# Kernel optimization log

Hardware: AMD Instinct MI355X
Metric: run time of the kernel (lower is better)

The kernel has to match this reference:

```python
import jax, jax.numpy as jnp
import numpy as np

N_NODES = 100000
N_EDGES = 1600000
IN_FEATS = 128
N_HIDDEN = 128
OUT_DIM = 32
BN_EPS = 1e-5


def setup_inputs() -> dict:
    key = jax.random.key(0)
    ks = jax.random.split(key, 12)
    s = 0.05  # weight init scale
    return {
        "features": jax.random.normal(ks[0], (N_NODES, IN_FEATS), dtype=jnp.float32),
        "src": jax.random.randint(ks[1], (N_EDGES,), 0, N_NODES),
        "dst": jax.random.randint(ks[2], (N_EDGES,), 0, N_NODES),
        # layer 0: in_feats -> n_hidden
        "Ws0": jax.random.normal(ks[3], (IN_FEATS, N_HIDDEN), dtype=jnp.float32) * s,
        "Wn0": jax.random.normal(ks[4], (IN_FEATS, N_HIDDEN), dtype=jnp.float32) * s,
        "b0": jnp.zeros((N_HIDDEN,), jnp.float32),
        # layer 1: n_hidden -> n_hidden
        "Ws1": jax.random.normal(ks[5], (N_HIDDEN, N_HIDDEN), dtype=jnp.float32) * s,
        "Wn1": jax.random.normal(ks[6], (N_HIDDEN, N_HIDDEN), dtype=jnp.float32) * s,
        "b1": jnp.zeros((N_HIDDEN,), jnp.float32),
        # layer 2 (output): n_hidden -> out_dim, no activation
        "Ws2": jax.random.normal(ks[7], (N_HIDDEN, OUT_DIM), dtype=jnp.float32) * s,
        "Wn2": jax.random.normal(ks[8], (N_HIDDEN, OUT_DIM), dtype=jnp.float32) * s,
        "b2": jnp.zeros((OUT_DIM,), jnp.float32),
        # batch norms after layers 0 and 1
        "g0": jnp.ones((N_HIDDEN,), jnp.float32),
        "be0": jnp.zeros((N_HIDDEN,), jnp.float32),
        "g1": jnp.ones((N_HIDDEN,), jnp.float32),
        "be1": jnp.zeros((N_HIDDEN,), jnp.float32),
    }


def _sage_mean(h, src, dst, inv_deg, Ws, Wn, b):
    # DGL SAGEConv('mean'): fc_self(h) + fc_neigh(mean of in-neighbor feats)
    agg = jax.ops.segment_sum(h[src], dst, num_segments=N_NODES) * inv_deg
    return h @ Ws + agg @ Wn + b


def _batch_norm(h, gamma, beta):
    mu = jnp.mean(h, axis=0)
    var = jnp.var(h, axis=0)
    return (h - mu) * jax.lax.rsqrt(var + BN_EPS) * gamma + beta


def reference(features, src, dst, Ws0, Wn0, b0, Ws1, Wn1, b1, Ws2, Wn2, b2, g0, be0, g1, be1):
    ones = jnp.ones((N_EDGES,), jnp.float32)
    deg = jax.ops.segment_sum(ones, dst, num_segments=N_NODES)
    inv_deg = (1.0 / jnp.maximum(deg, 1.0))[:, None]  # [N,1]

    # layer 0: SAGEConv internal activation, then BN + external activation
    h = jax.nn.relu(_sage_mean(features, src, dst, inv_deg, Ws0, Wn0, b0))
    h = jax.nn.relu(_batch_norm(h, g0, be0))
    # layer 1 (hidden)
    h = jax.nn.relu(_sage_mean(h, src, dst, inv_deg, Ws1, Wn1, b1))
    h = jax.nn.relu(_batch_norm(h, g1, be1))
    # layer 2 (output): no activation, no BN (idx > n_hidden_layers)
    h = _sage_mean(h, src, dst, inv_deg, Ws2, Wn2, b2)

    # dgl.mean_nodes over a single graph -> [1, out_dim], then softmax over classes
    hg = jnp.mean(h, axis=0, keepdims=True)
    return jax.nn.softmax(hg, axis=1)
```

## Files before the change

kernel.cpp:

```cpp
#include <hip/hip_runtime.h>
#include <hip/hip_bf16.h>

typedef __hip_bfloat16 bf16;
typedef __hip_bfloat162 bf162;

#define NN 100000
#define NE 1600000
#define BN_EPS 1e-5f

#define BSH 8
#define NBUCK ((NN + 255) >> BSH)
#define ABLK 128
#define EPBA ((NE + ABLK - 1) / ABLK)
#define CAP 6144

struct alignas(16) bf16x8 { bf16 v[8]; };

typedef __bf16 bfrag __attribute__((ext_vector_type(8)));
typedef float f4 __attribute__((ext_vector_type(4)));
typedef float f16v __attribute__((ext_vector_type(16)));
typedef float f2 __attribute__((ext_vector_type(2)));

static __device__ __forceinline__ float b2f(bf16 x){ return __bfloat162float(x); }
static __device__ __forceinline__ bf16 f2b(float x){ return __float2bfloat16(x); }

static __device__ __forceinline__ uint2 pk8_fp8(float x0,float x1,float x2,float x3,
                                                float x4,float x5,float x6,float x7)
{
    int lo = __builtin_amdgcn_cvt_pk_fp8_f32(x0, x1, 0, 0);
    lo = __builtin_amdgcn_cvt_pk_fp8_f32(x2, x3, lo, 1);
    int hi = __builtin_amdgcn_cvt_pk_fp8_f32(x4, x5, 0, 0);
    hi = __builtin_amdgcn_cvt_pk_fp8_f32(x6, x7, hi, 1);
    return make_uint2((unsigned)lo, (unsigned)hi);
}

__global__ __launch_bounds__(256) void k_convert(const float* __restrict__ in,
                                                 unsigned char* __restrict__ outf8, int n)
{
    int i = (blockIdx.x * 256 + threadIdx.x) * 8;
    if (i + 7 < n) {
        float4 a = *(const float4*)(in + i);
        float4 b = *(const float4*)(in + i + 4);
        *(uint2*)(outf8 + i) = pk8_fp8(a.x,a.y,a.z,a.w,b.x,b.y,b.z,b.w);
    }
}

__global__ __launch_bounds__(256) void k_wtrans(const float* __restrict__ W0, const float* __restrict__ W1,
                                                const float* __restrict__ W2, const float* __restrict__ W3,
                                                bf16* __restrict__ T0, bf16* __restrict__ T1,
                                                bf16* __restrict__ T2, bf16* __restrict__ T3)
{
    int m = blockIdx.x >> 6;
    int t = (blockIdx.x & 63) * 256 + threadIdx.x;
    const float* W = (m == 0) ? W0 : (m == 1) ? W1 : (m == 2) ? W2 : W3;
    bf16* T = (m == 0) ? T0 : (m == 1) ? T1 : (m == 2) ? T2 : T3;
    int j = t & 7;
    int lane = (t >> 3) & 63;
    int frag = t >> 9;
    int ks = frag >> 2, ct = frag & 3;
    int k = ks * 16 + (lane >> 5) * 8 + j;
    int n = ct * 32 + (lane & 31);
    T[t] = f2b(W[k * 128 + n]);
}

__global__ __launch_bounds__(256) void k_pa1(const int* __restrict__ dst, const int* __restrict__ src,
                                             int* __restrict__ bucketCountD, int* __restrict__ blockBaseD,
                                             int* __restrict__ bucketCountS, int* __restrict__ blockBaseS)
{
    __shared__ int histD[NBUCK];
    __shared__ int histS[NBUCK];
    int t = threadIdx.x;
    for (int i = t; i < NBUCK; i += 256) { histD[i] = 0; histS[i] = 0; }
    __syncthreads();
    int e0 = blockIdx.x * EPBA, e1 = min(e0 + EPBA, NE);
    for (int e = e0 + t; e < e1; e += 256) {
        unsigned bd = ((unsigned)dst[e]) >> BSH;
        unsigned bs = ((unsigned)src[e]) >> BSH;
        if (bd < (unsigned)NBUCK) atomicAdd(&histD[bd], 1);
        if (bs < (unsigned)NBUCK) atomicAdd(&histS[bs], 1);
    }
    __syncthreads();
    for (int i = t; i < NBUCK; i += 256) {
        blockBaseD[blockIdx.x * NBUCK + i] = atomicAdd(&bucketCountD[i], histD[i]);
        blockBaseS[blockIdx.x * NBUCK + i] = atomicAdd(&bucketCountS[i], histS[i]);
    }
}

__global__ __launch_bounds__(512) void k_bscan2(const int* __restrict__ cntD, int* __restrict__ startD,
                                                const int* __restrict__ cntS, int* __restrict__ startS)
{
    __shared__ int sd[512];
    const int* cnt = (blockIdx.x == 0) ? cntD : cntS;
    int* start = (blockIdx.x == 0) ? startD : startS;
    int t = threadIdx.x;
    int v = (t < NBUCK) ? cnt[t] : 0;
    sd[t] = v;
    __syncthreads();
    for (int o = 1; o < 512; o <<= 1) {
        int x = (t >= o) ? sd[t - o] : 0;
        __syncthreads();
        sd[t] += x;
        __syncthreads();
    }
    if (t < NBUCK) start[t] = sd[t] - v;
    if (t == 0) start[NBUCK] = NE;
}

__global__ __launch_bounds__(256) void k_pa2(const int* __restrict__ src, const int* __restrict__ dst,
                                             const int* __restrict__ bucketStartD, const int* __restrict__ blockBaseD,
                                             const int* __restrict__ bucketStartS, const int* __restrict__ blockBaseS,
                                             unsigned* __restrict__ packD, unsigned* __restrict__ packS)
{
    __shared__ int baseD[NBUCK];
    __shared__ int curD[NBUCK];
    __shared__ int baseS[NBUCK];
    __shared__ int curS[NBUCK];
    int t = threadIdx.x;
    for (int i = t; i < NBUCK; i += 256) {
        baseD[i] = bucketStartD[i] + blockBaseD[blockIdx.x * NBUCK + i];
        curD[i] = 0;
        baseS[i] = bucketStartS[i] + blockBaseS[blockIdx.x * NBUCK + i];
        curS[i] = 0;
    }
    __syncthreads();
    int e0 = blockIdx.x * EPBA, e1 = min(e0 + EPBA, NE);
    for (int e = e0 + t; e < e1; e += 256) {
        int s = src[e], d = dst[e];
        unsigned bd = ((unsigned)d) >> BSH;
        if (bd < (unsigned)NBUCK) {
            int r = atomicAdd(&curD[bd], 1);
            unsigned idx = (unsigned)(baseD[bd] + r);
            if (idx < (unsigned)NE)
                packD[idx] = (((unsigned)d & 255u) << 24) | ((unsigned)s & 0xFFFFFFu);
        }
        unsigned bs = ((unsigned)s) >> BSH;
        if (bs < (unsigned)NBUCK) {
            int r = atomicAdd(&curS[bs], 1);
            unsigned idx = (unsigned)(baseS[bs] + r);
            if (idx < (unsigned)NE)
                packS[idx] = (((unsigned)s & 255u) << 24) | ((unsigned)d & 0xFFFFFFu);
        }
    }
}

__global__ __launch_bounds__(256) void k_pbD(const unsigned* __restrict__ packD, const int* __restrict__ bucketStartD,
                                             int* __restrict__ offs, float* __restrict__ invd,
                                             int* __restrict__ esrc)
{
    __shared__ int dcnt[256];
    __shared__ int sscan[256];
    __shared__ int cur[256];
    __shared__ int S[CAP];
    int t = threadIdx.x;
    int b = blockIdx.x;
    int base = b << BSH;
    dcnt[t] = 0;
    cur[t] = 0;
    for (int i = t; i < CAP; i += 256) S[i] = 0;
    __syncthreads();
    int p0 = bucketStartD[b], p1 = bucketStartD[b + 1];
    int cnt = p1 - p0;
    for (int i = p0 + t; i < p1; i += 256)
        atomicAdd(&dcnt[packD[i] >> 24], 1);
    __syncthreads();
    int my = dcnt[t];
    sscan[t] = my;
    __syncthreads();
    for (int o = 1; o < 256; o <<= 1) {
        int v = (t >= o) ? sscan[t - o] : 0;
        __syncthreads();
        sscan[t] += v;
        __syncthreads();
    }
    int lo = sscan[t] - my;
    if (base + t < NN) {
        offs[base + t] = p0 + lo;
        invd[base + t] = 1.0f / (float)max(my, 1);
    }
    if (b == NBUCK - 1 && t == 0) offs[NN] = NE;
    __syncthreads();
    sscan[t] = lo;
    __syncthreads();
    if (cnt <= CAP) {
        for (int i = p0 + t; i < p1; i += 256) {
            unsigned v = packD[i];
            unsigned li = v >> 24;
            int pos = sscan[li] + atomicAdd(&cur[li], 1);
            if ((unsigned)pos >= (unsigned)cnt) pos = cnt - 1;
            S[pos] = (int)(v & 0xFFFFFFu);
        }
        __syncthreads();
        for (int i = t; i < cnt; i += 256) esrc[p0 + i] = S[i];
    } else {
        for (int i = p0 + t; i < p1; i += 256) {
            unsigned v = packD[i];
            unsigned li = v >> 24;
            int pos = sscan[li] + atomicAdd(&cur[li], 1);
            if ((unsigned)pos >= (unsigned)cnt) pos = cnt - 1;
            esrc[p0 + pos] = (int)(v & 0xFFFFFFu);
        }
    }
}

__global__ __launch_bounds__(256) void k_wsrc2(const unsigned* __restrict__ packS, const int* __restrict__ bucketStartS,
                                               const float* __restrict__ invd, float* __restrict__ wsrc)
{
    __shared__ float wacc[256];
    int t = threadIdx.x;
    wacc[t] = 0.f;
    __syncthreads();
    int b = blockIdx.x;
    int base = b << BSH;
    int p0 = bucketStartS[b], p1 = bucketStartS[b + 1];
    for (int i = p0 + t; i < p1; i += 256) {
        unsigned v = packS[i];
        unsigned li = v >> 24;
        unsigned dy = v & 0xFFFFFFu;
        if (dy >= (unsigned)NN) dy = 0u;
        atomicAdd(&wacc[li], invd[dy]);
    }
    __syncthreads();
    if (base + t < NN) wsrc[base + t] = wacc[t];
}

__global__ __launch_bounds__(256) void k_aggregate(const unsigned char* __restrict__ inf8, bf16* __restrict__ out,
                                                   const int* __restrict__ offs, const int* __restrict__ esrc,
                                                   const float* __restrict__ invd,
                                                   const float* __restrict__ scsh, int use_ss)
{
    int row = blockIdx.x * 4 + (threadIdx.x >> 6);
    if (row >= NN) return;
    int lane = threadIdx.x & 63;
    int grp = lane >> 4;
    int c0 = (lane & 15) * 8;
    float sc[8], sh[8];
    if (use_ss) {
#pragma unroll
        for (int j = 0; j < 8; j++) { sc[j] = scsh[c0 + j]; sh[j] = scsh[128 + c0 + j]; }
    }
    int e0 = offs[row], e1 = offs[row + 1];
    float a[8];
#pragma unroll
    for (int j = 0; j < 8; j++) a[j] = 0.f;

    auto unpack = [&](uint2 u, float* v) {
        f2 p0 = __builtin_amdgcn_cvt_pk_f32_fp8(u.x, 0);
        f2 p1 = __builtin_amdgcn_cvt_pk_f32_fp8(u.x, 1);
        f2 p2 = __builtin_amdgcn_cvt_pk_f32_fp8(u.y, 0);
        f2 p3 = __builtin_amdgcn_cvt_pk_f32_fp8(u.y, 1);
        v[0]=p0.x; v[1]=p0.y; v[2]=p1.x; v[3]=p1.y; v[4]=p2.x; v[5]=p2.y; v[6]=p3.x; v[7]=p3.y;
    };

    int e = e0 + grp;
    for (; e + 12 < e1; e += 16) {
        int s0 = esrc[e], s1 = esrc[e + 4], s2 = esrc[e + 8], s3 = esrc[e + 12];
        uint2 u0 = *(const uint2*)&inf8[(size_t)s0 * 128 + c0];
        uint2 u1 = *(const uint2*)&inf8[(size_t)s1 * 128 + c0];
        uint2 u2 = *(const uint2*)&inf8[(size_t)s2 * 128 + c0];
        uint2 u3 = *(const uint2*)&inf8[(size_t)s3 * 128 + c0];
        float v0[8], v1[8], v2[8], v3[8];
        unpack(u0, v0); unpack(u1, v1); unpack(u2, v2); unpack(u3, v3);
        if (use_ss) {
#pragma unroll
            for (int j = 0; j < 8; j++)
                a[j] += fmaxf(v0[j] * sc[j] + sh[j], 0.f) + fmaxf(v1[j] * sc[j] + sh[j], 0.f)
                      + fmaxf(v2[j] * sc[j] + sh[j], 0.f) + fmaxf(v3[j] * sc[j] + sh[j], 0.f);
        } else {
#pragma unroll
            for (int j = 0; j < 8; j++)
                a[j] += (v0[j] + v1[j]) + (v2[j] + v3[j]);
        }
    }
    if (e < e1) {
        int i1 = e + 4, i2 = e + 8;
        float m1 = (i1 < e1) ? 1.f : 0.f;
        float m2 = (i2 < e1) ? 1.f : 0.f;
        if (i1 >= e1) i1 = e;
        if (i2 >= e1) i2 = e;
        int s0 = esrc[e], s1 = esrc[i1], s2 = esrc[i2];
        uint2 u0 = *(const uint2*)&inf8[(size_t)s0 * 128 + c0];
        uint2 u1 = *(const uint2*)&inf8[(size_t)s1 * 128 + c0];
        uint2 u2 = *(const uint2*)&inf8[(size_t)s2 * 128 + c0];
        float v0[8], v1[8], v2[8];
        unpack(u0, v0); unpack(u1, v1); unpack(u2, v2);
        if (use_ss) {
#pragma unroll
            for (int j = 0; j < 8; j++)
                a[j] += fmaxf(v0[j] * sc[j] + sh[j], 0.f)
                      + m1 * fmaxf(v1[j] * sc[j] + sh[j], 0.f)
                      + m2 * fmaxf(v2[j] * sc[j] + sh[j], 0.f);
        } else {
#pragma unroll
            for (int j = 0; j < 8; j++)
                a[j] += v0[j] + m1 * v1[j] + m2 * v2[j];
        }
    }
#pragma unroll
    for (int j = 0; j < 8; j++) {
        a[j] += __shfl_xor(a[j], 16);
        a[j] += __shfl_xor(a[j], 32);
    }
    if (grp == 0) {
        float id = invd[row];
        bf16x8 o;
#pragma unroll
        for (int j = 0; j < 8; j++) o.v[j] = f2b(a[j] * id);
        *(bf16x8*)&out[(size_t)row * 128 + c0] = o;
    }
}

#define GM 128
__global__ __launch_bounds__(256, 4) void k_gemm_mfma(const void* __restrict__ HsSrc, int hs_fp8,
                                                      const bf16* __restrict__ Ag,
                                                      const bf16* __restrict__ Wst, const bf16* __restrict__ Wnt,
                                                      const float* __restrict__ bias,
                                                      const float* __restrict__ scsh, int use_ss,
                                                      bf16* __restrict__ outp, unsigned char* __restrict__ outf8,
                                                      float* __restrict__ bnsums)
{
    __shared__ bf16 sout[128][136];
    __shared__ float sredsum[128], sredsq[128];
    int t = threadIdx.x;
    int lane = t & 63;
    int l31 = lane & 31;
    int half = lane >> 5;
    int m0 = (t >> 6) * 32;
    int row0 = blockIdx.x * GM;

    if (t < 128) { sredsum[t] = 0.f; sredsq[t] = 0.f; }
    __syncthreads();

    int arow = row0 + m0 + l31;
    int gc = (arow < NN) ? arow : 0;

    f16v acc[4];
#pragma unroll
    for (int ct = 0; ct < 4; ct++)
#pragma unroll
        for (int r = 0; r < 16; r++) acc[ct][r] = 0.f;

#pragma unroll
    for (int ks = 0; ks < 8; ks++) {
        int k0 = ks * 16 + half * 8;

        bfrag aa = *(const bfrag*)&Ag[(size_t)gc * 128 + k0];
        bfrag ah;
        {
            float hv[8];
            if (hs_fp8) {
                uint2 u = *(const uint2*)((const unsigned char*)HsSrc + (size_t)gc * 128 + k0);
                f2 q0 = __builtin_amdgcn_cvt_pk_f32_fp8(u.x, 0);
                f2 q1 = __builtin_amdgcn_cvt_pk_f32_fp8(u.x, 1);
                f2 q2 = __builtin_amdgcn_cvt_pk_f32_fp8(u.y, 0);
                f2 q3 = __builtin_amdgcn_cvt_pk_f32_fp8(u.y, 1);
                hv[0]=q0.x; hv[1]=q0.y; hv[2]=q1.x; hv[3]=q1.y;
                hv[4]=q2.x; hv[5]=q2.y; hv[6]=q3.x; hv[7]=q3.y;
            } else {
                const float* fp = (const float*)HsSrc + (size_t)gc * 128 + k0;
                float4 x = *(const float4*)fp;
                float4 y = *(const float4*)(fp + 4);
                hv[0]=x.x; hv[1]=x.y; hv[2]=x.z; hv[3]=x.w;
                hv[4]=y.x; hv[5]=y.y; hv[6]=y.z; hv[7]=y.w;
            }
            if (use_ss) {
                float4 s0 = *(const float4*)&scsh[k0];
                float4 s1 = *(const float4*)&scsh[k0 + 4];
                float4 h0 = *(const float4*)&scsh[128 + k0];
                float4 h1 = *(const float4*)&scsh[128 + k0 + 4];
                hv[0] = fmaxf(hv[0]*s0.x + h0.x, 0.f); hv[1] = fmaxf(hv[1]*s0.y + h0.y, 0.f);
                hv[2] = fmaxf(hv[2]*s0.z + h0.z, 0.f); hv[3] = fmaxf(hv[3]*s0.w + h0.w, 0.f);
                hv[4] = fmaxf(hv[4]*s1.x + h1.x, 0.f); hv[5] = fmaxf(hv[5]*s1.y + h1.y, 0.f);
                hv[6] = fmaxf(hv[6]*s1.z + h1.z, 0.f); hv[7] = fmaxf(hv[7]*s1.w + h1.w, 0.f);
            }
#pragma unroll
            for (int j = 0; j < 8; j++) ah[j] = (__bf16)hv[j];
        }

#pragma unroll
        for (int ct = 0; ct < 4; ct++) {
            size_t fo = (size_t)((ks * 4 + ct) * 64 + lane) * 8;
            bfrag bs  = *(const bfrag*)&Wst[fo];
            bfrag bnf = *(const bfrag*)&Wnt[fo];
            acc[ct] = __builtin_amdgcn_mfma_f32_32x32x16_bf16(ah, bs,  acc[ct], 0, 0, 0);
            acc[ct] = __builtin_amdgcn_mfma_f32_32x32x16_bf16(aa, bnf, acc[ct], 0, 0, 0);
        }
    }

    float psum[4], psq[4];
#pragma unroll
    for (int ct = 0; ct < 4; ct++) {
        int col = ct * 32 + l31;
        float bv = bias[col];
        float s = 0.f, s2 = 0.f;
#pragma unroll
        for (int r = 0; r < 16; r++) {
            int lrow = m0 + 4 * half + (r & 3) + 8 * (r >> 2);
            float v = fmaxf(acc[ct][r] + bv, 0.f);
            sout[lrow][col] = f2b(v);
            if (row0 + lrow < NN) { s += v; s2 += v * v; }
        }
        psum[ct] = s; psq[ct] = s2;
    }
#pragma unroll
    for (int ct = 0; ct < 4; ct++) {
        psum[ct] += __shfl_xor(psum[ct], 32);
        psq[ct]  += __shfl_xor(psq[ct], 32);
    }
    if (lane < 32) {
#pragma unroll
        for (int ct = 0; ct < 4; ct++) {
            atomicAdd(&sredsum[ct * 32 + lane], psum[ct]);
            atomicAdd(&sredsq[ct * 32 + lane],  psq[ct]);
        }
    }

#pragma unroll
    for (int i = 0; i < 8; i++) {
        int idx = i * 64 + lane;
        int row = m0 + (idx >> 4);
        int c16 = idx & 15;
        int grow = row0 + row;
        if (grow < NN) {
            bf16x8 ov = *(const bf16x8*)&sout[row][c16 * 8];
            if (outp) *(bf16x8*)&outp[(size_t)grow * 128 + c16 * 8] = ov;
            if (outf8) {
                *(uint2*)&outf8[(size_t)grow * 128 + c16 * 8] =
                    pk8_fp8(b2f(ov.v[0]), b2f(ov.v[1]), b2f(ov.v[2]), b2f(ov.v[3]),
                            b2f(ov.v[4]), b2f(ov.v[5]), b2f(ov.v[6]), b2f(ov.v[7]));
            }
        }
    }

    __syncthreads();
    if (t < 128) {
        atomicAdd(&bnsums[t], sredsum[t]);
        atomicAdd(&bnsums[128 + t], sredsq[t]);
    }
}

__global__ void k_bn_fin(const float* __restrict__ sums, const float* __restrict__ g,
                         const float* __restrict__ be, float* __restrict__ scsh)
{
    int t = threadIdx.x;
    if (t < 128) {
        float mu = sums[t] / (float)NN;
        float var = sums[128 + t] / (float)NN - mu * mu;
        float sc = g[t] * rsqrtf(var + BN_EPS);
        scsh[t] = sc;
        scsh[128 + t] = be[t] - mu * sc;
    }
}

__global__ __launch_bounds__(256) void k_l2_reduce(const bf16* __restrict__ h, const float* __restrict__ scsh,
                                                   const float* __restrict__ wsrc, float* __restrict__ ue)
{
    __shared__ float su[128], se[128];
    int t = threadIdx.x;
    if (t < 128) { su[t] = 0.f; se[t] = 0.f; }
    __syncthreads();
    int c0 = (t & 15) * 8;
    int rof = t >> 4;
    float sc[8], sh[8];
#pragma unroll
    for (int j = 0; j < 8; j++) { sc[j] = scsh[c0 + j]; sh[j] = scsh[128 + c0 + j]; }
    float u[8], es[8];
#pragma unroll
    for (int j = 0; j < 8; j++) { u[j] = 0.f; es[j] = 0.f; }
    int rpb = (NN + gridDim.x - 1) / gridDim.x;
    int r0 = blockIdx.x * rpb;
    int r1 = min(r0 + rpb, NN);
    for (int r = r0 + rof; r < r1; r += 16) {
        bf16x8 v = *(const bf16x8*)&h[(size_t)r * 128 + c0];
        float w = wsrc[r];
#pragma unroll
        for (int j = 0; j < 8; j++) {
            float x = fmaxf(b2f(v.v[j]) * sc[j] + sh[j], 0.f);
            u[j] += x; es[j] += w * x;
        }
    }
#pragma unroll
    for (int j = 0; j < 8; j++) { atomicAdd(&su[c0 + j], u[j]); atomicAdd(&se[c0 + j], es[j]); }
    __syncthreads();
    if (t < 128) { atomicAdd(&ue[t], su[t]); atomicAdd(&ue[128 + t], se[t]); }
}

__global__ void k_final(const float* __restrict__ ue, const float* __restrict__ Ws2,
                        const float* __restrict__ Wn2, const float* __restrict__ b2,
                        float* __restrict__ out)
{
    __shared__ float logit[32];
    int t = threadIdx.x;
    const float inv = 1.0f / (float)NN;
    if (t < 32) {
        float acc = b2[t];
        for (int k = 0; k < 128; k++)
            acc += (ue[k] * inv) * Ws2[k * 32 + t] + (ue[128 + k] * inv) * Wn2[k * 32 + t];
        logit[t] = acc;
    }
    __syncthreads();
    if (t < 32) {
        float m = -1e30f;
        for (int j = 0; j < 32; j++) m = fmaxf(m, logit[j]);
        float s = 0.f;
        for (int j = 0; j < 32; j++) s += expf(logit[j] - m);
        out[t] = expf(logit[t] - m) / s;
    }
}

extern "C" void kernel_launch(void* const* d_in, const int* in_sizes, int n_in,
                              void* d_out, int out_size, void* d_ws, size_t ws_size,
                              hipStream_t stream)
{
    const float* feat = (const float*)d_in[0];
    const int*   src  = (const int*)d_in[1];
    const int*   dst  = (const int*)d_in[2];
    const float* Ws0  = (const float*)d_in[3];
    const float* Wn0  = (const float*)d_in[4];
    const float* b0   = (const float*)d_in[5];
    const float* Ws1  = (const float*)d_in[6];
    const float* Wn1  = (const float*)d_in[7];
    const float* b1   = (const float*)d_in[8];
    const float* Ws2  = (const float*)d_in[9];
    const float* Wn2  = (const float*)d_in[10];
    const float* b2   = (const float*)d_in[11];
    const float* g0   = (const float*)d_in[12];
    const float* be0  = (const float*)d_in[13];
    const float* g1   = (const float*)d_in[14];
    const float* be1  = (const float*)d_in[15];

    char* p = (char*)d_ws;
    auto alloc = [&](size_t b) -> void* {
        void* r = (void*)p;
        p += (b + 255) & ~(size_t)255;
        return r;
    };
    bf16* A      = (bf16*)alloc((size_t)NN * 128 * 2);
    unsigned char* F8 = (unsigned char*)alloc((size_t)NN * 128);
    unsigned* packS = (unsigned*)alloc((size_t)NE * 4);
    int*  esrc   = (int*)alloc((size_t)NE * 4);
    int*  offs   = (int*)alloc((size_t)(NN + 1) * 4);
    float* invd  = (float*)alloc((size_t)NN * 4);
    float* wsrc  = (float*)alloc((size_t)NN * 4);
    char* zstart = p;
    int*  bucketCountD = (int*)alloc((NBUCK + 1) * 4);
    int*  bucketCountS = (int*)alloc((NBUCK + 1) * 4);
    float* bn0   = (float*)alloc(256 * 4);
    float* bn1   = (float*)alloc(256 * 4);
    float* ue    = (float*)alloc(256 * 4);
    size_t zlen = (size_t)(p - zstart);
    float* scsh0 = (float*)alloc(256 * 4);
    float* scsh1 = (float*)alloc(256 * 4);
    bf16* Ws0t   = (bf16*)alloc(16384 * 2);
    bf16* Wn0t   = (bf16*)alloc(16384 * 2);
    bf16* Ws1t   = (bf16*)alloc(16384 * 2);
    bf16* Wn1t   = (bf16*)alloc(16384 * 2);
    int*  bucketStartD = (int*)alloc((NBUCK + 1) * 4);
    int*  bucketStartS = (int*)alloc((NBUCK + 1) * 4);
    int*  blockBaseD   = (int*)alloc((size_t)ABLK * NBUCK * 4);
    int*  blockBaseS   = (int*)alloc((size_t)ABLK * NBUCK * 4);

    unsigned* packD = (unsigned*)A;

    hipMemsetAsync(zstart, 0, zlen, stream);

    const int GB = (NN + GM - 1) / GM;

    k_convert<<<(NN * 128) / (256 * 8), 256, 0, stream>>>(feat, F8, NN * 128);
    k_wtrans<<<256, 256, 0, stream>>>(Ws0, Wn0, Ws1, Wn1, Ws0t, Wn0t, Ws1t, Wn1t);

    k_pa1<<<ABLK, 256, 0, stream>>>(dst, src, bucketCountD, blockBaseD, bucketCountS, blockBaseS);
    k_bscan2<<<2, 512, 0, stream>>>(bucketCountD, bucketStartD, bucketCountS, bucketStartS);
    k_pa2<<<ABLK, 256, 0, stream>>>(src, dst, bucketStartD, blockBaseD, bucketStartS, blockBaseS, packD, packS);
    k_pbD<<<NBUCK, 256, 0, stream>>>(packD, bucketStartD, offs, invd, esrc);
    k_wsrc2<<<NBUCK, 256, 0, stream>>>(packS, bucketStartS, invd, wsrc);

    k_aggregate<<<(NN + 3) / 4, 256, 0, stream>>>(F8, A, offs, esrc, invd, nullptr, 0);
    k_gemm_mfma<<<GB, 256, 0, stream>>>(feat, 0, A, Ws0t, Wn0t, b0, nullptr, 0, nullptr, F8, bn0);
    k_bn_fin<<<1, 128, 0, stream>>>(bn0, g0, be0, scsh0);

    k_aggregate<<<(NN + 3) / 4, 256, 0, stream>>>(F8, A, offs, esrc, invd, scsh0, 1);
    k_gemm_mfma<<<GB, 256, 0, stream>>>(F8, 1, A, Ws1t, Wn1t, b1, scsh0, 1, A, nullptr, bn1);
    k_bn_fin<<<1, 128, 0, stream>>>(bn1, g1, be1, scsh1);

    k_l2_reduce<<<256, 256, 0, stream>>>(A, scsh1, wsrc, ue);
    k_final<<<1, 64, 0, stream>>>(ue, Ws2, Wn2, b2, (float*)d_out);
}
```

Before: 437.7 us.

## Fuse neighbor mean aggregation into the MFMA GEMM via shared memory

Merges the separate aggregation kernel into the GEMM kernel: each wave gathers and averages neighbor rows for its 32 rows into shared memory, then feeds them straight into the MFMA. This removes the bf16 aggregate write and read through global memory and one launch per layer. A second fp8 buffer is added so layer 0 output does not overwrite the features still being gathered. The risks are lower occupancy (launch bounds drop from 4 to 3 blocks per CU, and self-feature fragments are held in registers) and less parallelism in the gather, since each wave now handles 32 rows one after another, and 128-row blocks are fewer than the old per-row grid.

Result: slower. 460.5 us (+5.2%).

```diff
diff --git a/kernel.cpp b/kernel.cpp
--- a/kernel.cpp
+++ b/kernel.cpp
@@ -223,25 +223,36 @@
     if (base + t < NN) wsrc[base + t] = wacc[t];
 }
 
-__global__ __launch_bounds__(256) void k_aggregate(const unsigned char* __restrict__ inf8, bf16* __restrict__ out,
-                                                   const int* __restrict__ offs, const int* __restrict__ esrc,
-                                                   const float* __restrict__ invd,
-                                                   const float* __restrict__ scsh, int use_ss)
-{
-    int row = blockIdx.x * 4 + (threadIdx.x >> 6);
-    if (row >= NN) return;
-    int lane = threadIdx.x & 63;
+#define GM 128
+__global__ __launch_bounds__(256, 3) void k_gemm_fused(const void* __restrict__ HsSrc, int hs_fp8,
+                                                       const unsigned char* __restrict__ Gf8,
+                                                       const int* __restrict__ offs, const int* __restrict__ esrc,
+                                                       const float* __restrict__ invd,
+                                                       const bf16* __restrict__ Wst, const bf16* __restrict__ Wnt,
+                                                       const float* __restrict__ bias,
+                                                       const float* __restrict__ scsh, int use_ss,
+                                                       bf16* __restrict__ outp, unsigned char* __restrict__ outf8,
+                                                       float* __restrict__ bnsums)
+{
+    __shared__ bf16 sout[128][136];
+    __shared__ float sredsum[128], sredsq[128];
+    int t = threadIdx.x;
+    int lane = t & 63;
+    int l31 = lane & 31;
+    int half = lane >> 5;
+    int l16 = lane & 15;
     int grp = lane >> 4;
-    int c0 = (lane & 15) * 8;
-    float sc[8], sh[8];
+    int m0 = (t >> 6) * 32;
+    int row0 = blockIdx.x * GM;
+
+    if (t < 128) { sredsum[t] = 0.f; sredsq[t] = 0.f; }
+
+    int c0 = l16 * 8;
+    float gsc[8], gsh[8];
     if (use_ss) {
 #pragma unroll
-        for (int j = 0; j < 8; j++) { sc[j] = scsh[c0 + j]; sh[j] = scsh[128 + c0 + j]; }
-    }
-    int e0 = offs[row], e1 = offs[row + 1];
-    float a[8];
-#pragma unroll
-    for (int j = 0; j < 8; j++) a[j] = 0.f;
+        for (int j = 0; j < 8; j++) { gsc[j] = scsh[c0 + j]; gsh[j] = scsh[128 + c0 + j]; }
+    }
 
     auto unpack = [&](uint2 u, float* v) {
         f2 p0 = __builtin_amdgcn_cvt_pk_f32_fp8(u.x, 0);
@@ -251,117 +262,91 @@
         v[0]=p0.x; v[1]=p0.y; v[2]=p1.x; v[3]=p1.y; v[4]=p2.x; v[5]=p2.y; v[6]=p3.x; v[7]=p3.y;
     };
 
-    int e = e0 + grp;
-    for (; e + 12 < e1; e += 16) {
-        int s0 = esrc[e], s1 = esrc[e + 4], s2 = esrc[e + 8], s3 = esrc[e + 12];
-        uint2 u0 = *(const uint2*)&inf8[(size_t)s0 * 128 + c0];
-        uint2 u1 = *(const uint2*)&inf8[(size_t)s1 * 128 + c0];
-        uint2 u2 = *(const uint2*)&inf8[(size_t)s2 * 128 + c0];
-        uint2 u3 = *(const uint2*)&inf8[(size_t)s3 * 128 + c0];
-        float v0[8], v1[8], v2[8], v3[8];
-        unpack(u0, v0); unpack(u1, v1); unpack(u2, v2); unpack(u3, v3);
-        if (use_ss) {
-#pragma unroll
-            for (int j = 0; j < 8; j++)
-                a[j] += fmaxf(v0[j] * sc[j] + sh[j], 0.f) + fmaxf(v1[j] * sc[j] + sh[j], 0.f)
-                      + fmaxf(v2[j] * sc[j] + sh[j], 0.f) + fmaxf(v3[j] * sc[j] + sh[j], 0.f);
-        } else {
-#pragma unroll
-            for (int j = 0; j < 8; j++)
-                a[j] += (v0[j] + v1[j]) + (v2[j] + v3[j]);
-        }
-    }
-    if (e < e1) {
-        int i1 = e + 4, i2 = e + 8;
-        float m1 = (i1 < e1) ? 1.f : 0.f;
-        float m2 = (i2 < e1) ? 1.f : 0.f;
-        if (i1 >= e1) i1 = e;
-        if (i2 >= e1) i2 = e;
-        int s0 = esrc[e], s1 = esrc[i1], s2 = esrc[i2];
-        uint2 u0 = *(const uint2*)&inf8[(size_t)s0 * 128 + c0];
-        uint2 u1 = *(const uint2*)&inf8[(size_t)s1 * 128 + c0];
-        uint2 u2 = *(const uint2*)&inf8[(size_t)s2 * 128 + c0];
-        float v0[8], v1[8], v2[8];
-        unpack(u0, v0); unpack(u1, v1); unpack(u2, v2);
-        if (use_ss) {
-#pragma unroll
-            for (int j = 0; j < 8; j++)
-                a[j] += fmaxf(v0[j] * sc[j] + sh[j], 0.f)
-                      + m1 * fmaxf(v1[j] * sc[j] + sh[j], 0.f)
-                      + m2 * fmaxf(v2[j] * sc[j] + sh[j], 0.f);
-        } else {
-#pragma unroll
-            for (int j = 0; j < 8; j++)
-                a[j] += v0[j] + m1 * v1[j] + m2 * v2[j];
-        }
-    }
-#pragma unroll
-    for (int j = 0; j < 8; j++) {
-        a[j] += __shfl_xor(a[j], 16);
-        a[j] += __shfl_xor(a[j], 32);
-    }
-    if (grp == 0) {
-        float id = invd[row];
-        bf16x8 o;
-#pragma unroll
-        for (int j = 0; j < 8; j++) o.v[j] = f2b(a[j] * id);
-        *(bf16x8*)&out[(size_t)row * 128 + c0] = o;
-    }
-}
-
-#define GM 128
-__global__ __launch_bounds__(256, 4) void k_gemm_mfma(const void* __restrict__ HsSrc, int hs_fp8,
-                                                      const bf16* __restrict__ Ag,
-                                                      const bf16* __restrict__ Wst, const bf16* __restrict__ Wnt,
-                                                      const float* __restrict__ bias,
-                                                      const float* __restrict__ scsh, int use_ss,
-                                                      bf16* __restrict__ outp, unsigned char* __restrict__ outf8,
-                                                      float* __restrict__ bnsums)
-{
-    __shared__ bf16 sout[128][136];
-    __shared__ float sredsum[128], sredsq[128];
-    int t = threadIdx.x;
-    int lane = t & 63;
-    int l31 = lane & 31;
-    int half = lane >> 5;
-    int m0 = (t >> 6) * 32;
-    int row0 = blockIdx.x * GM;
-
-    if (t < 128) { sredsum[t] = 0.f; sredsq[t] = 0.f; }
-    __syncthreads();
+    for (int rr = 0; rr < 32; rr++) {
+        int grow = row0 + m0 + rr;
+        if (grow < NN) {
+            int e0 = offs[grow], e1 = offs[grow + 1];
+            float a[8];
+#pragma unroll
+            for (int j = 0; j < 8; j++) a[j] = 0.f;
+
+            int e = e0 + grp;
+            for (; e + 12 < e1; e += 16) {
+                int s0 = esrc[e], s1 = esrc[e + 4], s2 = esrc[e + 8], s3 = esrc[e + 12];
+                uint2 u0 = *(const uint2*)&Gf8[(size_t)s0 * 128 + c0];
+                uint2 u1 = *(const uint2*)&Gf8[(size_t)s1 * 128 + c0];
+                uint2 u2 = *(const uint2*)&Gf8[(size_t)s2 * 128 + c0];
+                uint2 u3 = *(const uint2*)&Gf8[(size_t)s3 * 128 + c0];
+                float v0[8], v1[8], v2[8], v3[8];
+                unpack(u0, v0); unpack(u1, v1); unpack(u2, v2); unpack(u3, v3);
+                if (use_ss) {
+#pragma unroll
+                    for (int j = 0; j < 8; j++)
+                        a[j] += fmaxf(v0[j] * gsc[j] + gsh[j], 0.f) + fmaxf(v1[j] * gsc[j] + gsh[j], 0.f)
+                              + fmaxf(v2[j] * gsc[j] + gsh[j], 0.f) + fmaxf(v3[j] * gsc[j] + gsh[j], 0.f);
+                } else {
+#pragma unroll
+                    for (int j = 0; j < 8; j++)
+                        a[j] += (v0[j] + v1[j]) + (v2[j] + v3[j]);
+                }
+            }
+            if (e < e1) {
+                int i1 = e + 4, i2 = e + 8;
+                float m1 = (i1 < e1) ? 1.f : 0.f;
+                float m2 = (i2 < e1) ? 1.f : 0.f;
+                if (i1 >= e1) i1 = e;
+                if (i2 >= e1) i2 = e;
+                int s0 = esrc[e], s1 = esrc[i1], s2 = esrc[i2];
+                uint2 u0 = *(const uint2*)&Gf8[(size_t)s0 * 128 + c0];
+                uint2 u1 = *(const uint2*)&Gf8[(size_t)s1 * 128 + c0];
+                uint2 u2 = *(const uint2*)&Gf8[(size_t)s2 * 128 + c0];
+                float v0[8], v1[8], v2[8];
+                unpack(u0, v0); unpack(u1, v1); unpack(u2, v2);
+                if (use_ss) {
+#pragma unroll
+                    for (int j = 0; j < 8; j++)
+                        a[j] += fmaxf(v0[j] * gsc[j] + gsh[j], 0.f)
+                              + m1 * fmaxf(v1[j] * gsc[j] + gsh[j], 0.f)
+                              + m2 * fmaxf(v2[j] * gsc[j] + gsh[j], 0.f);
+                } else {
+#pragma unroll
+                    for (int j = 0; j < 8; j++)
+                        a[j] += v0[j] + m1 * v1[j] + m2 * v2[j];
+                }
+            }
+#pragma unroll
+            for (int j = 0; j < 8; j++) {
+                a[j] += __shfl_xor(a[j], 16);
+                a[j] += __shfl_xor(a[j], 32);
+            }
+            if (grp == 0) {
+                float id = invd[grow];
+                bf16x8 o;
+#pragma unroll
+                for (int j = 0; j < 8; j++) o.v[j] = f2b(a[j] * id);
+                *(bf16x8*)&sout[m0 + rr][c0] = o;
+            }
+        } else if (grp == 0) {
+            bf16x8 o;
+#pragma unroll
+            for (int j = 0; j < 8; j++) o.v[j] = f2b(0.f);
+            *(bf16x8*)&sout[m0 + rr][c0] = o;
+        }
+    }
 
     int arow = row0 + m0 + l31;
     int gc = (arow < NN) ? arow : 0;
-
-    f16v acc[4];
-#pragma unroll
-    for (int ct = 0; ct < 4; ct++)
-#pragma unroll
-        for (int r = 0; r < 16; r++) acc[ct][r] = 0.f;
-
-#pragma unroll
-    for (int ks = 0; ks < 8; ks++) {
-        int k0 = ks * 16 + half * 8;
-
-        bfrag aa = *(const bfrag*)&Ag[(size_t)gc * 128 + k0];
-        bfrag ah;
-        {
-            float hv[8];
-            if (hs_fp8) {
-                uint2 u = *(const uint2*)((const unsigned char*)HsSrc + (size_t)gc * 128 + k0);
-                f2 q0 = __builtin_amdgcn_cvt_pk_f32_fp8(u.x, 0);
-                f2 q1 = __builtin_amdgcn_cvt_pk_f32_fp8(u.x, 1);
-                f2 q2 = __builtin_amdgcn_cvt_pk_f32_fp8(u.y, 0);
-                f2 q3 = __builtin_amdgcn_cvt_pk_f32_fp8(u.y, 1);
-                hv[0]=q0.x; hv[1]=q0.y; hv[2]=q1.x; hv[3]=q1.y;
-                hv[4]=q2.x; hv[5]=q2.y; hv[6]=q3.x; hv[7]=q3.y;
-            } else {
-                const float* fp = (const float*)HsSrc + (size_t)gc * 128 + k0;
-                float4 x = *(const float4*)fp;
-                float4 y = *(const float4*)(fp + 4);
-                hv[0]=x.x; hv[1]=x.y; hv[2]=x.z; hv[3]=x.w;
-                hv[4]=y.x; hv[5]=y.y; hv[6]=y.z; hv[7]=y.w;
-            }
+    bfrag ah[8];
+    if (hs_fp8) {
+#pragma unroll
+        for (int ks = 0; ks < 8; ks++) {
+            int k0 = ks * 16 + half * 8;
+            uint2 u = *(const uint2*)((const unsigned char*)HsSrc + (size_t)gc * 128 + k0);
+            f2 q0 = __builtin_amdgcn_cvt_pk_f32_fp8(u.x, 0);
+            f2 q1 = __builtin_amdgcn_cvt_pk_f32_fp8(u.x, 1);
+            f2 q2 = __builtin_amdgcn_cvt_pk_f32_fp8(u.y, 0);
+            f2 q3 = __builtin_amdgcn_cvt_pk_f32_fp8(u.y, 1);
+            float hv[8] = {q0.x,q0.y,q1.x,q1.y,q2.x,q2.y,q3.x,q3.y};
             if (use_ss) {
                 float4 s0 = *(const float4*)&scsh[k0];
                 float4 s1 = *(const float4*)&scsh[k0 + 4];
@@ -372,16 +357,53 @@
                 hv[4] = fmaxf(hv[4]*s1.x + h1.x, 0.f); hv[5] = fmaxf(hv[5]*s1.y + h1.y, 0.f);
                 hv[6] = fmaxf(hv[6]*s1.z + h1.z, 0.f); hv[7] = fmaxf(hv[7]*s1.w + h1.w, 0.f);
             }
-#pragma unroll
-            for (int j = 0; j < 8; j++) ah[j] = (__bf16)hv[j];
-        }
-
+            bfrag f;
+#pragma unroll
+            for (int j = 0; j < 8; j++) f[j] = (__bf16)hv[j];
+            ah[ks] = f;
+        }
+    } else {
+#pragma unroll
+        for (int ks = 0; ks < 8; ks++) {
+            int k0 = ks * 16 + half * 8;
+            const float* fp = (const float*)HsSrc + (size_t)gc * 128 + k0;
+            float4 x = *(const float4*)fp;
+            float4 y = *(const float4*)(fp + 4);
+            float hv[8] = {x.x,x.y,x.z,x.w,y.x,y.y,y.z,y.w};
+            if (use_ss) {
+                float4 s0 = *(const float4*)&scsh[k0];
+                float4 s1 = *(const float4*)&scsh[k0 + 4];
+                float4 h0 = *(const float4*)&scsh[128 + k0];
+                float4 h1 = *(const float4*)&scsh[128 + k0 + 4];
+                hv[0] = fmaxf(hv[0]*s0.x + h0.x, 0.f); hv[1] = fmaxf(hv[1]*s0.y + h0.y, 0.f);
+                hv[2] = fmaxf(hv[2]*s0.z + h0.z, 0.f); hv[3] = fmaxf(hv[3]*s0.w + h0.w, 0.f);
+                hv[4] = fmaxf(hv[4]*s1.x + h1.x, 0.f); hv[5] = fmaxf(hv[5]*s1.y + h1.y, 0.f);
+                hv[6] = fmaxf(hv[6]*s1.z + h1.z, 0.f); hv[7] = fmaxf(hv[7]*s1.w + h1.w, 0.f);
+            }
+            bfrag f;
+#pragma unroll
+            for (int j = 0; j < 8; j++) f[j] = (__bf16)hv[j];
+            ah[ks] = f;
+        }
+    }
+
+    __syncthreads();
+
+    f16v acc[4];
+#pragma unroll
+    for (int ct = 0; ct < 4; ct++)
+#pragma unroll
+        for (int r = 0; r < 16; r++) acc[ct][r] = 0.f;
+
+#pragma unroll
+    for (int ks = 0; ks < 8; ks++) {
+        bfrag aa = *(const bfrag*)&sout[m0 + l31][ks * 16 + half * 8];
 #pragma unroll
         for (int ct = 0; ct < 4; ct++) {
             size_t fo = (size_t)((ks * 4 + ct) * 64 + lane) * 8;
             bfrag bs  = *(const bfrag*)&Wst[fo];
             bfrag bnf = *(const bfrag*)&Wnt[fo];
-            acc[ct] = __builtin_amdgcn_mfma_f32_32x32x16_bf16(ah, bs,  acc[ct], 0, 0, 0);
+            acc[ct] = __builtin_amdgcn_mfma_f32_32x32x16_bf16(ah[ks], bs,  acc[ct], 0, 0, 0);
             acc[ct] = __builtin_amdgcn_mfma_f32_32x32x16_bf16(aa, bnf, acc[ct], 0, 0, 0);
         }
     }
@@ -535,7 +557,8 @@
         return r;
     };
     bf16* A      = (bf16*)alloc((size_t)NN * 128 * 2);
-    unsigned char* F8 = (unsigned char*)alloc((size_t)NN * 128);
+    unsigned char* F8  = (unsigned char*)alloc((size_t)NN * 128);
+    unsigned char* F8b = (unsigned char*)alloc((size_t)NN * 128);
     unsigned* packS = (unsigned*)alloc((size_t)NE * 4);
     int*  esrc   = (int*)alloc((size_t)NE * 4);
     int*  offs   = (int*)alloc((size_t)(NN + 1) * 4);
@@ -574,12 +597,12 @@
     k_pbD<<<NBUCK, 256, 0, stream>>>(packD, bucketStartD, offs, invd, esrc);
     k_wsrc2<<<NBUCK, 256, 0, stream>>>(packS, bucketStartS, invd, wsrc);
 
-    k_aggregate<<<(NN + 3) / 4, 256, 0, stream>>>(F8, A, offs, esrc, invd, nullptr, 0);
-    k_gemm_mfma<<<GB, 256, 0, stream>>>(feat, 0, A, Ws0t, Wn0t, b0, nullptr, 0, nullptr, F8, bn0);
+    k_gemm_fused<<<GB, 256, 0, stream>>>(feat, 0, F8, offs, esrc, invd,
+                                         Ws0t, Wn0t, b0, nullptr, 0, nullptr, F8b, bn0);
     k_bn_fin<<<1, 128, 0, stream>>>(bn0, g0, be0, scsh0);
 
-    k_aggregate<<<(NN + 3) / 4, 256, 0, stream>>>(F8, A, offs, esrc, invd, scsh0, 1);
-    k_gemm_mfma<<<GB, 256, 0, stream>>>(F8, 1, A, Ws1t, Wn1t, b1, scsh0, 1, A, nullptr, bn1);
+    k_gemm_fused<<<GB, 256, 0, stream>>>(F8b, 1, F8b, offs, esrc, invd,
+                                         Ws1t, Wn1t, b1, scsh0, 1, A, nullptr, bn1);
     k_bn_fin<<<1, 128, 0, stream>>>(bn1, g1, be1, scsh1);
 
     k_l2_reduce<<<256, 256, 0, stream>>>(A, scsh1, wsrc, ue);
```

## Compute per-source weight sums via global atomics in dst-bucket pass, dropping src bucketing

Applied to the files above, without the earlier changes.

Removes the entire source-side bucket sort (histogram, scan, scatter to packS, and the k_wsrc2 reduction). Each source's sum of 1/deg(dst) is now accumulated with global float atomicAdds inside k_pbD while it processes dst buckets, and the wsrc buffer is zeroed by the existing memset. This cuts a full pass of edge reads and writes plus one kernel launch. In exchange it adds 1.6M scattered global atomics and makes the float sum order nondeterministic.

Result: slower. 495.5 us (+13.2%).

```diff
diff --git a/kernel.cpp b/kernel.cpp
--- a/kernel.cpp
+++ b/kernel.cpp
@@ -63,35 +63,26 @@
     T[t] = f2b(W[k * 128 + n]);
 }
 
-__global__ __launch_bounds__(256) void k_pa1(const int* __restrict__ dst, const int* __restrict__ src,
-                                             int* __restrict__ bucketCountD, int* __restrict__ blockBaseD,
-                                             int* __restrict__ bucketCountS, int* __restrict__ blockBaseS)
+__global__ __launch_bounds__(256) void k_pa1(const int* __restrict__ dst,
+                                             int* __restrict__ bucketCountD, int* __restrict__ blockBaseD)
 {
     __shared__ int histD[NBUCK];
-    __shared__ int histS[NBUCK];
-    int t = threadIdx.x;
-    for (int i = t; i < NBUCK; i += 256) { histD[i] = 0; histS[i] = 0; }
+    int t = threadIdx.x;
+    for (int i = t; i < NBUCK; i += 256) histD[i] = 0;
     __syncthreads();
     int e0 = blockIdx.x * EPBA, e1 = min(e0 + EPBA, NE);
     for (int e = e0 + t; e < e1; e += 256) {
         unsigned bd = ((unsigned)dst[e]) >> BSH;
-        unsigned bs = ((unsigned)src[e]) >> BSH;
         if (bd < (unsigned)NBUCK) atomicAdd(&histD[bd], 1);
-        if (bs < (unsigned)NBUCK) atomicAdd(&histS[bs], 1);
-    }
-    __syncthreads();
-    for (int i = t; i < NBUCK; i += 256) {
+    }
+    __syncthreads();
+    for (int i = t; i < NBUCK; i += 256)
         blockBaseD[blockIdx.x * NBUCK + i] = atomicAdd(&bucketCountD[i], histD[i]);
-        blockBaseS[blockIdx.x * NBUCK + i] = atomicAdd(&bucketCountS[i], histS[i]);
-    }
-}
-
-__global__ __launch_bounds__(512) void k_bscan2(const int* __restrict__ cntD, int* __restrict__ startD,
-                                                const int* __restrict__ cntS, int* __restrict__ startS)
+}
+
+__global__ __launch_bounds__(512) void k_bscan(const int* __restrict__ cnt, int* __restrict__ start)
 {
     __shared__ int sd[512];
-    const int* cnt = (blockIdx.x == 0) ? cntD : cntS;
-    int* start = (blockIdx.x == 0) ? startD : startS;
     int t = threadIdx.x;
     int v = (t < NBUCK) ? cnt[t] : 0;
     sd[t] = v;
@@ -108,19 +99,14 @@
 
 __global__ __launch_bounds__(256) void k_pa2(const int* __restrict__ src, const int* __restrict__ dst,
                                              const int* __restrict__ bucketStartD, const int* __restrict__ blockBaseD,
-                                             const int* __restrict__ bucketStartS, const int* __restrict__ blockBaseS,
-                                             unsigned* __restrict__ packD, unsigned* __restrict__ packS)
+                                             unsigned* __restrict__ packD)
 {
     __shared__ int baseD[NBUCK];
     __shared__ int curD[NBUCK];
-    __shared__ int baseS[NBUCK];
-    __shared__ int curS[NBUCK];
     int t = threadIdx.x;
     for (int i = t; i < NBUCK; i += 256) {
         baseD[i] = bucketStartD[i] + blockBaseD[blockIdx.x * NBUCK + i];
         curD[i] = 0;
-        baseS[i] = bucketStartS[i] + blockBaseS[blockIdx.x * NBUCK + i];
-        curS[i] = 0;
     }
     __syncthreads();
     int e0 = blockIdx.x * EPBA, e1 = min(e0 + EPBA, NE);
@@ -133,23 +119,17 @@
             if (idx < (unsigned)NE)
                 packD[idx] = (((unsigned)d & 255u) << 24) | ((unsigned)s & 0xFFFFFFu);
         }
-        unsigned bs = ((unsigned)s) >> BSH;
-        if (bs < (unsigned)NBUCK) {
-            int r = atomicAdd(&curS[bs], 1);
-            unsigned idx = (unsigned)(baseS[bs] + r);
-            if (idx < (unsigned)NE)
-                packS[idx] = (((unsigned)s & 255u) << 24) | ((unsigned)d & 0xFFFFFFu);
-        }
     }
 }
 
 __global__ __launch_bounds__(256) void k_pbD(const unsigned* __restrict__ packD, const int* __restrict__ bucketStartD,
                                              int* __restrict__ offs, float* __restrict__ invd,
-                                             int* __restrict__ esrc)
+                                             int* __restrict__ esrc, float* __restrict__ wsrc)
 {
     __shared__ int dcnt[256];
     __shared__ int sscan[256];
     __shared__ int cur[256];
+    __shared__ float sinvd[256];
     __shared__ int S[CAP];
     int t = threadIdx.x;
     int b = blockIdx.x;
@@ -173,9 +153,11 @@
         __syncthreads();
     }
     int lo = sscan[t] - my;
+    float iv = 1.0f / (float)max(my, 1);
+    sinvd[t] = iv;
     if (base + t < NN) {
         offs[base + t] = p0 + lo;
-        invd[base + t] = 1.0f / (float)max(my, 1);
+        invd[base + t] = iv;
     }
     if (b == NBUCK - 1 && t == 0) offs[NN] = NE;
     __syncthreads();
@@ -185,9 +167,11 @@
         for (int i = p0 + t; i < p1; i += 256) {
             unsigned v = packD[i];
             unsigned li = v >> 24;
+            int sval = (int)(v & 0xFFFFFFu);
             int pos = sscan[li] + atomicAdd(&cur[li], 1);
             if ((unsigned)pos >= (unsigned)cnt) pos = cnt - 1;
-            S[pos] = (int)(v & 0xFFFFFFu);
+            S[pos] = sval;
+            if ((unsigned)sval < (unsigned)NN) atomicAdd(&wsrc[sval], sinvd[li]);
         }
         __syncthreads();
         for (int i = t; i < cnt; i += 256) esrc[p0 + i] = S[i];
@@ -195,32 +179,13 @@
         for (int i = p0 + t; i < p1; i += 256) {
             unsigned v = packD[i];
             unsigned li = v >> 24;
+            int sval = (int)(v & 0xFFFFFFu);
             int pos = sscan[li] + atomicAdd(&cur[li], 1);
             if ((unsigned)pos >= (unsigned)cnt) pos = cnt - 1;
-            esrc[p0 + pos] = (int)(v & 0xFFFFFFu);
-        }
-    }
-}
-
-__global__ __launch_bounds__(256) void k_wsrc2(const unsigned* __restrict__ packS, const int* __restrict__ bucketStartS,
-                                               const float* __restrict__ invd, float* __restrict__ wsrc)
-{
-    __shared__ float wacc[256];
-    int t = threadIdx.x;
-    wacc[t] = 0.f;
-    __syncthreads();
-    int b = blockIdx.x;
-    int base = b << BSH;
-    int p0 = bucketStartS[b], p1 = bucketStartS[b + 1];
-    for (int i = p0 + t; i < p1; i += 256) {
-        unsigned v = packS[i];
-        unsigned li = v >> 24;
-        unsigned dy = v & 0xFFFFFFu;
-        if (dy >= (unsigned)NN) dy = 0u;
-        atomicAdd(&wacc[li], invd[dy]);
-    }
-    __syncthreads();
-    if (base + t < NN) wsrc[base + t] = wacc[t];
+            esrc[p0 + pos] = sval;
+            if ((unsigned)sval < (unsigned)NN) atomicAdd(&wsrc[sval], sinvd[li]);
+        }
+    }
 }
 
 __global__ __launch_bounds__(256) void k_aggregate(const unsigned char* __restrict__ inf8, bf16* __restrict__ out,
@@ -536,14 +501,12 @@
     };
     bf16* A      = (bf16*)alloc((size_t)NN * 128 * 2);
     unsigned char* F8 = (unsigned char*)alloc((size_t)NN * 128);
-    unsigned* packS = (unsigned*)alloc((size_t)NE * 4);
     int*  esrc   = (int*)alloc((size_t)NE * 4);
     int*  offs   = (int*)alloc((size_t)(NN + 1) * 4);
     float* invd  = (float*)alloc((size_t)NN * 4);
+    char* zstart = p;
     float* wsrc  = (float*)alloc((size_t)NN * 4);
-    char* zstart = p;
     int*  bucketCountD = (int*)alloc((NBUCK + 1) * 4);
-    int*  bucketCountS = (int*)alloc((NBUCK + 1) * 4);
     float* bn0   = (float*)alloc(256 * 4);
     float* bn1   = (float*)alloc(256 * 4);
     float* ue    = (float*)alloc(256 * 4);
@@ -555,9 +518,7 @@
     bf16* Ws1t   = (bf16*)alloc(16384 * 2);
     bf16* Wn1t   = (bf16*)alloc(16384 * 2);
     int*  bucketStartD = (int*)alloc((NBUCK + 1) * 4);
-    int*  bucketStartS = (int*)alloc((NBUCK + 1) * 4);
     int*  blockBaseD   = (int*)alloc((size_t)ABLK * NBUCK * 4);
-    int*  blockBaseS   = (int*)alloc((size_t)ABLK * NBUCK * 4);
 
     unsigned* packD = (unsigned*)A;
 
@@ -568,11 +529,10 @@
     k_convert<<<(NN * 128) / (256 * 8), 256, 0, stream>>>(feat, F8, NN * 128);
     k_wtrans<<<256, 256, 0, stream>>>(Ws0, Wn0, Ws1, Wn1, Ws0t, Wn0t, Ws1t, Wn1t);
 
-    k_pa1<<<ABLK, 256, 0, stream>>>(dst, src, bucketCountD, blockBaseD, bucketCountS, blockBaseS);
-    k_bscan2<<<2, 512, 0, stream>>>(bucketCountD, bucketStartD, bucketCountS, bucketStartS);
-    k_pa2<<<ABLK, 256, 0, stream>>>(src, dst, bucketStartD, blockBaseD, bucketStartS, blockBaseS, packD, packS);
-    k_pbD<<<NBUCK, 256, 0, stream>>>(packD, bucketStartD, offs, invd, esrc);
-    k_wsrc2<<<NBUCK, 256, 0, stream>>>(packS, bucketStartS, invd, wsrc);
+    k_pa1<<<ABLK, 256, 0, stream>>>(dst, bucketCountD, blockBaseD);
+    k_bscan<<<1, 512, 0, stream>>>(bucketCountD, bucketStartD);
+    k_pa2<<<ABLK, 256, 0, stream>>>(src, dst, bucketStartD, blockBaseD, packD);
+    k_pbD<<<NBUCK, 256, 0, stream>>>(packD, bucketStartD, offs, invd, esrc, wsrc);
 
     k_aggregate<<<(NN + 3) / 4, 256, 0, stream>>>(F8, A, offs, esrc, invd, nullptr, 0);
     k_gemm_mfma<<<GB, 256, 0, stream>>>(feat, 0, A, Ws0t, Wn0t, b0, nullptr, 0, nullptr, F8, bn0);
```
